# Kernel optimization log

Hardware: AMD Instinct MI355X
Metric: run time of the kernel (lower is better)

Reference implementation:

```python
import jax, jax.numpy as jnp
import numpy as np

WINDOW = 12  # fixed half-window from the original module


def setup_inputs() -> dict:
    key = jax.random.key(0)
    ks = jax.random.split(key, 8)
    B, S, G, H = 8, 512, 16, 128
    Da, Dm = 8 * H, 2 * H
    att = jax.random.normal(ks[0], (B, S, Da), jnp.float32)
    mod = jax.random.normal(ks[1], (B, S, Dm), jnp.float32)
    W_att = jax.random.normal(ks[2], (3 * Da,), jnp.float32) * 0.02
    b_att = jax.random.normal(ks[3], (1,), jnp.float32) * 0.02
    W_mod = jax.random.normal(ks[4], (3 * Dm,), jnp.float32) * 0.02
    b_mod = jax.random.normal(ks[5], (1,), jnp.float32) * 0.02
    q_enc = jax.random.normal(ks[6], (B, 30, Dm), jnp.float32)
    gap_indices = jax.random.randint(ks[7], (B, G), 0, S)
    mask = jnp.ones((B, S), jnp.int32)
    q_mask = jnp.ones((B, 30), jnp.int32)
    return dict(att=att, mod=mod, W_att=W_att, b_att=b_att, W_mod=W_mod,
                b_mod=b_mod, q_enc=q_enc, gap_indices=gap_indices,
                mask=mask, q_mask=q_mask)


def _pools(x, maskf, wmf):
    # x: [B,S,D]; maskf: [B,S] float; wmf: [B,G-1,S] float window masks
    # gap 0: full-sequence pooling (max is unmasked, avg divides by mask sum -- faithful)
    max0 = jnp.max(x, axis=1)                                   # [B,D]
    avg0 = jnp.sum(x, axis=1) / jnp.sum(maskf, axis=1, keepdims=True)
    p0 = jnp.concatenate([max0, avg0], axis=-1)[:, None, :]      # [B,1,2D]
    # remaining gaps: masked windowed max/avg (masked entries zeroed, as in torch)
    s = jnp.einsum('bgs,bsd->bgd', wmf, x)                       # windowed sums
    cnt = jnp.sum(wmf, axis=2, keepdims=True)                    # [B,G-1,1]
    avg = s / cnt
    mx = jnp.max(x[:, None, :, :] * wmf[:, :, :, None], axis=2)  # [B,G-1,D]
    return jnp.concatenate([p0, jnp.concatenate([mx, avg], axis=-1)], axis=1)


def reference(att, mod, W_att, b_att, W_mod, b_mod, q_enc, gap_indices, mask, q_mask):
    B, S, _ = mod.shape
    bidx = jnp.arange(B)[:, None]
    att_gaps = att[bidx, gap_indices]   # [B,G,Da]
    mod_gaps = mod[bidx, gap_indices]   # [B,G,Dm]

    maskf = mask.astype(jnp.float32)
    gaps_rest = gap_indices[:, 1:]      # [B,G-1]
    idx = jnp.arange(S)
    wm = ((idx[None, None, :] >= gaps_rest[:, :, None] - WINDOW)
          & (idx[None, None, :] <= gaps_rest[:, :, None] + WINDOW)
          & (mask[:, None, :] > 0))
    wmf = wm.astype(jnp.float32)        # [B,G-1,S]

    pools_att = _pools(att, maskf, wmf)  # [B,G,2*Da]
    pools_mod = _pools(mod, maskf, wmf)  # [B,G,2*Dm]

    att_cat = jnp.concatenate([att_gaps, pools_att], axis=-1)  # [B,G,3*Da]
    mod_cat = jnp.concatenate([mod_gaps, pools_mod], axis=-1)  # [B,G,3*Dm]

    logits = (jnp.einsum('bgd,d->bg', att_cat, W_att) + b_att
              + jnp.einsum('bgd,d->bg', mod_cat, W_mod) + b_mod)
    return logits  # [B,G]
```

## Files before the change

### kernel.cpp

```cpp
#include <hip/hip_runtime.h>
#include <hip/hip_bf16.h>
#include <math.h>

#define B 8
#define S 512
#define G 16
#define DA 1024
#define DM 256
#define WIN 12
#define NCHUNK 32
#define ROWS (S / NCHUNK)
#define DTOT (DA + DM)
#define NW 8
#define RPW (ROWS / NW)

__inline__ __device__ float4 fmax4(float4 a, float4 b) {
    return make_float4(fmaxf(a.x, b.x), fmaxf(a.y, b.y),
                       fmaxf(a.z, b.z), fmaxf(a.w, b.w));
}
__inline__ __device__ float dot4(float4 a, float4 b) {
    return a.x * b.x + a.y * b.y + a.z * b.z + a.w * b.w;
}

__inline__ __device__ float4 blockReduceSum4_16(float4 v, float4* sh) {
    int lane = threadIdx.x & 63, w = threadIdx.x >> 6;
#pragma unroll
    for (int o = 32; o > 0; o >>= 1) {
        v.x += __shfl_xor(v.x, o, 64);
        v.y += __shfl_xor(v.y, o, 64);
        v.z += __shfl_xor(v.z, o, 64);
        v.w += __shfl_xor(v.w, o, 64);
    }
    __syncthreads();
    if (lane == 0) sh[w] = v;
    __syncthreads();
    float4 r = sh[0];
#pragma unroll
    for (int ww = 1; ww < 16; ++ww) {
        r.x += sh[ww].x; r.y += sh[ww].y; r.z += sh[ww].z; r.w += sh[ww].w;
    }
    return r;
}

__inline__ __device__ float blockReduceSum_16(float v, float* sh) {
    int lane = threadIdx.x & 63, w = threadIdx.x >> 6;
#pragma unroll
    for (int o = 32; o > 0; o >>= 1) v += __shfl_xor(v, o, 64);
    __syncthreads();
    if (lane == 0) sh[w] = v;
    __syncthreads();
    float r = sh[0];
#pragma unroll
    for (int ww = 1; ww < 16; ++ww) r += sh[ww];
    return r;
}

__global__ __launch_bounds__(512) void k_fused(
    const float* __restrict__ att, const float* __restrict__ mod,
    const float* __restrict__ Wa, const float* __restrict__ Wm,
    float* __restrict__ proj0a, float* __restrict__ proj2a,
    float* __restrict__ proj0m, float* __restrict__ proj2m,
    float* __restrict__ pmax)
{
    __shared__ float part[NW][DTOT];
    const int ch = blockIdx.x, b = blockIdx.y;
    const int t = threadIdx.x, lane = t & 63, w = t >> 6;

    const float4* W0 = (const float4*)Wa;
    const float4* W2 = (const float4*)(Wa + 2 * DA);
    float4 w0[4], w2[4];
#pragma unroll
    for (int k = 0; k < 4; ++k) {
        w0[k] = W0[lane + 64 * k];
        w2[k] = W2[lane + 64 * k];
    }
    const float4 wq0 = ((const float4*)Wm)[lane];
    const float4 wq2 = ((const float4*)(Wm + 2 * DM))[lane];

    float4 amax[4], mmax;
#pragma unroll
    for (int k = 0; k < 4; ++k)
        amax[k] = make_float4(-INFINITY, -INFINITY, -INFINITY, -INFINITY);
    mmax = make_float4(-INFINITY, -INFINITY, -INFINITY, -INFINITY);

    const int srow0 = ch * ROWS + w * RPW;
#pragma unroll
    for (int r = 0; r < RPW; ++r) {
        const int row = b * S + srow0 + r;
        const float4* arow = (const float4*)(att + (size_t)row * DA);
        float p0 = 0.f, p2 = 0.f;
#pragma unroll
        for (int k = 0; k < 4; ++k) {
            float4 va = arow[lane + 64 * k];
            p0 += dot4(va, w0[k]);
            p2 += dot4(va, w2[k]);
            amax[k] = fmax4(amax[k], va);
        }
        float4 vm = ((const float4*)(mod + (size_t)row * DM))[lane];
        float q0 = dot4(vm, wq0);
        float q2 = dot4(vm, wq2);
        mmax = fmax4(mmax, vm);

#pragma unroll
        for (int o = 32; o > 0; o >>= 1) {
            p0 += __shfl_xor(p0, o, 64);
            p2 += __shfl_xor(p2, o, 64);
            q0 += __shfl_xor(q0, o, 64);
            q2 += __shfl_xor(q2, o, 64);
        }
        if (lane == 0) {
            proj0a[row] = p0;
            proj2a[row] = p2;
            proj0m[row] = q0;
            proj2m[row] = q2;
        }
    }

    float4* pr = (float4*)&part[w][0];
#pragma unroll
    for (int k = 0; k < 4; ++k) pr[lane + 64 * k] = amax[k];
    ((float4*)&part[w][DA])[lane] = mmax;
    __syncthreads();

    for (int d = t; d < DTOT; d += 512) {
        float m = part[0][d];
#pragma unroll
        for (int ww = 1; ww < NW; ++ww) m = fmaxf(m, part[ww][d]);
        pmax[((size_t)b * NCHUNK + ch) * DTOT + d] = m;
    }
}

__global__ __launch_bounds__(1024) void k_final(
    const float* __restrict__ att, const float* __restrict__ mod,
    const float* __restrict__ Wa, const float* __restrict__ Wm,
    const float* __restrict__ ba, const float* __restrict__ bm,
    const int* __restrict__ gidx, const int* __restrict__ mask,
    const float* __restrict__ proj0a, const float* __restrict__ proj2a,
    const float* __restrict__ proj0m, const float* __restrict__ proj2m,
    const float* __restrict__ pmax,
    float* __restrict__ out)
{
    __shared__ float4 s4v[16];
    __shared__ float s16[16];
    __shared__ float4 pA[4][256];
    __shared__ float  pM[4][256];
    const int g = blockIdx.x, b = blockIdx.y, t = threadIdx.x;
    const int gi = gidx[b * G + g];

    if (g == 0) {
        float sa = 0.f, sm = 0.f, cm = 0.f;
        for (int s = t; s < S; s += 1024) {
            sa += proj2a[b * S + s];
            sm += proj2m[b * S + s];
            cm += (float)mask[b * S + s];
        }
        float gm = 0.f;
        for (int d = t; d < DTOT; d += 1024) {
            float m = -INFINITY;
#pragma unroll
            for (int ch = 0; ch < NCHUNK; ++ch)
                m = fmaxf(m, pmax[((size_t)b * NCHUNK + ch) * DTOT + d]);
            float wgt = (d < DA) ? Wa[DA + d] : Wm[DM + (d - DA)];
            gm += wgt * m;
        }
        float4 r = blockReduceSum4_16(make_float4(sa, sm, cm, gm), s4v);
        if (t == 0) {
            float res = proj0a[b * S + gi] + proj0m[b * S + gi] + r.w +
                        r.x / r.z + r.y / r.z + ba[0] + bm[0];
            out[b * G + 0] = res;
        }
    } else {
        int lo = gi - WIN; if (lo < 0) lo = 0;
        int hi = gi + WIN; if (hi > S - 1) hi = S - 1;

        const int sb = t >> 8;
        const int dt = t & 255;

        float4 m4 = make_float4(0.f, 0.f, 0.f, 0.f);
        float mm = 0.f, sa = 0.f, sm = 0.f, cn = 0.f;
        const float4* a4 = (const float4*)att;
        for (int s = lo + sb; s <= hi; s += 4) {
            if (mask[b * S + s] > 0) {
                float4 v = a4[(size_t)(b * S + s) * (DA / 4) + dt];
                m4 = fmax4(m4, v);
                mm = fmaxf(mm, mod[(size_t)(b * S + s) * DM + dt]);
                if (dt == 0) {
                    sa += proj2a[b * S + s];
                    sm += proj2m[b * S + s];
                    cn += 1.f;
                }
            }
        }
        pA[sb][dt] = m4;
        pM[sb][dt] = mm;
        __syncthreads();

        float pa = 0.f, pm = 0.f;
        if (t < 256) {
            float4 mm4 = fmax4(fmax4(pA[0][t], pA[1][t]),
                               fmax4(pA[2][t], pA[3][t]));
            float mmm = fmaxf(fmaxf(pM[0][t], pM[1][t]),
                              fmaxf(pM[2][t], pM[3][t]));
            const float4* W1a4 = (const float4*)(Wa + DA);
            pa = dot4(mm4, W1a4[t]);
            pm = Wm[DM + t] * mmm;
        }
        float4 r = blockReduceSum4_16(make_float4(pa, pm, sa, sm), s4v);
        cn = blockReduceSum_16(cn, s16);
        if (t == 0) {
            float res = proj0a[b * S + gi] + proj0m[b * S + gi] +
                        r.x + r.y + r.z / cn + r.w / cn + ba[0] + bm[0];
            out[b * G + g] = res;
        }
    }
}

extern "C" void kernel_launch(void* const* d_in, const int* in_sizes, int n_in,
                              void* d_out, int out_size, void* d_ws, size_t ws_size,
                              hipStream_t stream) {
    const float* att  = (const float*)d_in[0];
    const float* mod  = (const float*)d_in[1];
    const float* Wa   = (const float*)d_in[2];
    const float* ba   = (const float*)d_in[3];
    const float* Wm   = (const float*)d_in[4];
    const float* bm   = (const float*)d_in[5];
    const int* gidx   = (const int*)d_in[7];
    const int* mask   = (const int*)d_in[8];
    float* out = (float*)d_out;

    float* ws     = (float*)d_ws;
    float* proj0a = ws;
    float* proj2a = proj0a + B * S;
    float* proj0m = proj2a + B * S;
    float* proj2m = proj0m + B * S;
    float* pmax   = proj2m + B * S;

    k_fused<<<dim3(NCHUNK, B), 512, 0, stream>>>(att, mod, Wa, Wm,
                                                 proj0a, proj2a, proj0m, proj2m,
                                                 pmax);
    k_final<<<dim3(G, B), 1024, 0, stream>>>(att, mod, Wa, Wm, ba, bm, gidx, mask,
                                             proj0a, proj2a, proj0m, proj2m,
                                             pmax, out);
}
```

Measured before the change: 18.87 us.

## Merge two kernels into one cooperative launch with a grid-wide sync

Fuses the per-chunk projection/max kernel and the per-gap finalization kernel into one cooperative kernel separated by a grid sync, so the second launch and its gap go away. The second phase now runs on 128 of the 256 blocks with 512 threads each and reuses the shared buffer, reorganizing the window max by wavefront rows. This adds the cost of a grid-wide barrier and requires all 256 blocks to be co-resident, which the cooperative launch needs.

```diff
diff --git a/kernel.cpp b/kernel.cpp
--- a/kernel.cpp
+++ b/kernel.cpp
@@ -1,6 +1,8 @@
 #include <hip/hip_runtime.h>
-#include <hip/hip_bf16.h>
+#include <hip/hip_cooperative_groups.h>
 #include <math.h>
+
+namespace cg = cooperative_groups;
 
 #define B 8
 #define S 512
@@ -22,7 +24,7 @@
     return a.x * b.x + a.y * b.y + a.z * b.z + a.w * b.w;
 }
 
-__inline__ __device__ float4 blockReduceSum4_16(float4 v, float4* sh) {
+__inline__ __device__ float4 blockReduceSum4_8(float4 v, float4* sh) {
     int lane = threadIdx.x & 63, w = threadIdx.x >> 6;
 #pragma unroll
     for (int o = 32; o > 0; o >>= 1) {
@@ -36,126 +38,108 @@
     __syncthreads();
     float4 r = sh[0];
 #pragma unroll
-    for (int ww = 1; ww < 16; ++ww) {
+    for (int ww = 1; ww < NW; ++ww) {
         r.x += sh[ww].x; r.y += sh[ww].y; r.z += sh[ww].z; r.w += sh[ww].w;
     }
     return r;
 }
 
-__inline__ __device__ float blockReduceSum_16(float v, float* sh) {
-    int lane = threadIdx.x & 63, w = threadIdx.x >> 6;
-#pragma unroll
-    for (int o = 32; o > 0; o >>= 1) v += __shfl_xor(v, o, 64);
-    __syncthreads();
-    if (lane == 0) sh[w] = v;
-    __syncthreads();
-    float r = sh[0];
-#pragma unroll
-    for (int ww = 1; ww < 16; ++ww) r += sh[ww];
-    return r;
-}
-
-__global__ __launch_bounds__(512) void k_fused(
-    const float* __restrict__ att, const float* __restrict__ mod,
-    const float* __restrict__ Wa, const float* __restrict__ Wm,
-    float* __restrict__ proj0a, float* __restrict__ proj2a,
-    float* __restrict__ proj0m, float* __restrict__ proj2m,
-    float* __restrict__ pmax)
-{
-    __shared__ float part[NW][DTOT];
-    const int ch = blockIdx.x, b = blockIdx.y;
-    const int t = threadIdx.x, lane = t & 63, w = t >> 6;
-
-    const float4* W0 = (const float4*)Wa;
-    const float4* W2 = (const float4*)(Wa + 2 * DA);
-    float4 w0[4], w2[4];
-#pragma unroll
-    for (int k = 0; k < 4; ++k) {
-        w0[k] = W0[lane + 64 * k];
-        w2[k] = W2[lane + 64 * k];
-    }
-    const float4 wq0 = ((const float4*)Wm)[lane];
-    const float4 wq2 = ((const float4*)(Wm + 2 * DM))[lane];
-
-    float4 amax[4], mmax;
-#pragma unroll
-    for (int k = 0; k < 4; ++k)
-        amax[k] = make_float4(-INFINITY, -INFINITY, -INFINITY, -INFINITY);
-    mmax = make_float4(-INFINITY, -INFINITY, -INFINITY, -INFINITY);
-
-    const int srow0 = ch * ROWS + w * RPW;
-#pragma unroll
-    for (int r = 0; r < RPW; ++r) {
-        const int row = b * S + srow0 + r;
-        const float4* arow = (const float4*)(att + (size_t)row * DA);
-        float p0 = 0.f, p2 = 0.f;
-#pragma unroll
-        for (int k = 0; k < 4; ++k) {
-            float4 va = arow[lane + 64 * k];
-            p0 += dot4(va, w0[k]);
-            p2 += dot4(va, w2[k]);
-            amax[k] = fmax4(amax[k], va);
-        }
-        float4 vm = ((const float4*)(mod + (size_t)row * DM))[lane];
-        float q0 = dot4(vm, wq0);
-        float q2 = dot4(vm, wq2);
-        mmax = fmax4(mmax, vm);
-
-#pragma unroll
-        for (int o = 32; o > 0; o >>= 1) {
-            p0 += __shfl_xor(p0, o, 64);
-            p2 += __shfl_xor(p2, o, 64);
-            q0 += __shfl_xor(q0, o, 64);
-            q2 += __shfl_xor(q2, o, 64);
-        }
-        if (lane == 0) {
-            proj0a[row] = p0;
-            proj2a[row] = p2;
-            proj0m[row] = q0;
-            proj2m[row] = q2;
-        }
-    }
-
-    float4* pr = (float4*)&part[w][0];
-#pragma unroll
-    for (int k = 0; k < 4; ++k) pr[lane + 64 * k] = amax[k];
-    ((float4*)&part[w][DA])[lane] = mmax;
-    __syncthreads();
-
-    for (int d = t; d < DTOT; d += 512) {
-        float m = part[0][d];
-#pragma unroll
-        for (int ww = 1; ww < NW; ++ww) m = fmaxf(m, part[ww][d]);
-        pmax[((size_t)b * NCHUNK + ch) * DTOT + d] = m;
-    }
-}
-
-__global__ __launch_bounds__(1024) void k_final(
+__global__ __launch_bounds__(512) void k_all(
     const float* __restrict__ att, const float* __restrict__ mod,
     const float* __restrict__ Wa, const float* __restrict__ Wm,
     const float* __restrict__ ba, const float* __restrict__ bm,
     const int* __restrict__ gidx, const int* __restrict__ mask,
-    const float* __restrict__ proj0a, const float* __restrict__ proj2a,
-    const float* __restrict__ proj0m, const float* __restrict__ proj2m,
-    const float* __restrict__ pmax,
-    float* __restrict__ out)
+    float* __restrict__ proj0a, float* __restrict__ proj2a,
+    float* __restrict__ proj0m, float* __restrict__ proj2m,
+    float* __restrict__ pmax, float* __restrict__ out)
 {
-    __shared__ float4 s4v[16];
-    __shared__ float s16[16];
-    __shared__ float4 pA[4][256];
-    __shared__ float  pM[4][256];
-    const int g = blockIdx.x, b = blockIdx.y, t = threadIdx.x;
+    __shared__ float part[NW][DTOT];
+    __shared__ float4 s4[NW];
+    const int t = threadIdx.x, lane = t & 63, w = t >> 6;
+
+    {
+        const int ch = blockIdx.x, b = blockIdx.y;
+
+        const float4* W0 = (const float4*)Wa;
+        const float4* W2 = (const float4*)(Wa + 2 * DA);
+        float4 w0[4], w2[4];
+#pragma unroll
+        for (int k = 0; k < 4; ++k) {
+            w0[k] = W0[lane + 64 * k];
+            w2[k] = W2[lane + 64 * k];
+        }
+        const float4 wq0 = ((const float4*)Wm)[lane];
+        const float4 wq2 = ((const float4*)(Wm + 2 * DM))[lane];
+
+        float4 amax[4], mmax;
+#pragma unroll
+        for (int k = 0; k < 4; ++k)
+            amax[k] = make_float4(-INFINITY, -INFINITY, -INFINITY, -INFINITY);
+        mmax = make_float4(-INFINITY, -INFINITY, -INFINITY, -INFINITY);
+
+        const int srow0 = ch * ROWS + w * RPW;
+#pragma unroll
+        for (int r = 0; r < RPW; ++r) {
+            const int row = b * S + srow0 + r;
+            const float4* arow = (const float4*)(att + (size_t)row * DA);
+            float p0 = 0.f, p2 = 0.f;
+#pragma unroll
+            for (int k = 0; k < 4; ++k) {
+                float4 va = arow[lane + 64 * k];
+                p0 += dot4(va, w0[k]);
+                p2 += dot4(va, w2[k]);
+                amax[k] = fmax4(amax[k], va);
+            }
+            float4 vm = ((const float4*)(mod + (size_t)row * DM))[lane];
+            float q0 = dot4(vm, wq0);
+            float q2 = dot4(vm, wq2);
+            mmax = fmax4(mmax, vm);
+
+#pragma unroll
+            for (int o = 32; o > 0; o >>= 1) {
+                p0 += __shfl_xor(p0, o, 64);
+                p2 += __shfl_xor(p2, o, 64);
+                q0 += __shfl_xor(q0, o, 64);
+                q2 += __shfl_xor(q2, o, 64);
+            }
+            if (lane == 0) {
+                proj0a[row] = p0;
+                proj2a[row] = p2;
+                proj0m[row] = q0;
+                proj2m[row] = q2;
+            }
+        }
+
+        float4* pr = (float4*)&part[w][0];
+#pragma unroll
+        for (int k = 0; k < 4; ++k) pr[lane + 64 * k] = amax[k];
+        ((float4*)&part[w][DA])[lane] = mmax;
+        __syncthreads();
+
+        for (int d = t; d < DTOT; d += 512) {
+            float m = part[0][d];
+#pragma unroll
+            for (int ww = 1; ww < NW; ++ww) m = fmaxf(m, part[ww][d]);
+            pmax[((size_t)b * NCHUNK + ch) * DTOT + d] = m;
+        }
+    }
+
+    cg::this_grid().sync();
+
+    const int bid = blockIdx.y * NCHUNK + blockIdx.x;
+    if (bid >= B * G) return;
+    const int g = bid & (G - 1), b = bid >> 4;
     const int gi = gidx[b * G + g];
 
     if (g == 0) {
         float sa = 0.f, sm = 0.f, cm = 0.f;
-        for (int s = t; s < S; s += 1024) {
+        for (int s = t; s < S; s += 512) {
             sa += proj2a[b * S + s];
             sm += proj2m[b * S + s];
             cm += (float)mask[b * S + s];
         }
         float gm = 0.f;
-        for (int d = t; d < DTOT; d += 1024) {
+        for (int d = t; d < DTOT; d += 512) {
             float m = -INFINITY;
 #pragma unroll
             for (int ch = 0; ch < NCHUNK; ++ch)
@@ -163,54 +147,55 @@
             float wgt = (d < DA) ? Wa[DA + d] : Wm[DM + (d - DA)];
             gm += wgt * m;
         }
-        float4 r = blockReduceSum4_16(make_float4(sa, sm, cm, gm), s4v);
+        float4 r = blockReduceSum4_8(make_float4(sa, sm, cm, gm), s4);
         if (t == 0) {
-            float res = proj0a[b * S + gi] + proj0m[b * S + gi] + r.w +
-                        r.x / r.z + r.y / r.z + ba[0] + bm[0];
-            out[b * G + 0] = res;
+            out[b * G + 0] = proj0a[b * S + gi] + proj0m[b * S + gi] + r.w +
+                             r.x / r.z + r.y / r.z + ba[0] + bm[0];
         }
     } else {
         int lo = gi - WIN; if (lo < 0) lo = 0;
         int hi = gi + WIN; if (hi > S - 1) hi = S - 1;
 
-        const int sb = t >> 8;
-        const int dt = t & 255;
-
-        float4 m4 = make_float4(0.f, 0.f, 0.f, 0.f);
-        float mm = 0.f, sa = 0.f, sm = 0.f, cn = 0.f;
-        const float4* a4 = (const float4*)att;
-        for (int s = lo + sb; s <= hi; s += 4) {
+        float4 amax2[4];
+#pragma unroll
+        for (int k = 0; k < 4; ++k) amax2[k] = make_float4(0.f, 0.f, 0.f, 0.f);
+        float4 mmax2 = make_float4(0.f, 0.f, 0.f, 0.f);
+        float sa = 0.f, sm = 0.f, cn = 0.f;
+
+        for (int s = lo + w; s <= hi; s += NW) {
             if (mask[b * S + s] > 0) {
-                float4 v = a4[(size_t)(b * S + s) * (DA / 4) + dt];
-                m4 = fmax4(m4, v);
-                mm = fmaxf(mm, mod[(size_t)(b * S + s) * DM + dt]);
-                if (dt == 0) {
-                    sa += proj2a[b * S + s];
-                    sm += proj2m[b * S + s];
+                const int row = b * S + s;
+                const float4* arow = (const float4*)(att + (size_t)row * DA);
+#pragma unroll
+                for (int k = 0; k < 4; ++k)
+                    amax2[k] = fmax4(amax2[k], arow[lane + 64 * k]);
+                mmax2 = fmax4(mmax2, ((const float4*)(mod + (size_t)row * DM))[lane]);
+                if (lane == 0) {
+                    sa += proj2a[row];
+                    sm += proj2m[row];
                     cn += 1.f;
                 }
             }
         }
-        pA[sb][dt] = m4;
-        pM[sb][dt] = mm;
+
+        float4* pr = (float4*)&part[w][0];
+#pragma unroll
+        for (int k = 0; k < 4; ++k) pr[lane + 64 * k] = amax2[k];
+        ((float4*)&part[w][DA])[lane] = mmax2;
         __syncthreads();
 
-        float pa = 0.f, pm = 0.f;
-        if (t < 256) {
-            float4 mm4 = fmax4(fmax4(pA[0][t], pA[1][t]),
-                               fmax4(pA[2][t], pA[3][t]));
-            float mmm = fmaxf(fmaxf(pM[0][t], pM[1][t]),
-                              fmaxf(pM[2][t], pM[3][t]));
-            const float4* W1a4 = (const float4*)(Wa + DA);
-            pa = dot4(mm4, W1a4[t]);
-            pm = Wm[DM + t] * mmm;
-        }
-        float4 r = blockReduceSum4_16(make_float4(pa, pm, sa, sm), s4v);
-        cn = blockReduceSum_16(cn, s16);
+        float wdot = 0.f;
+        for (int d = t; d < DTOT; d += 512) {
+            float m = part[0][d];
+#pragma unroll
+            for (int ww = 1; ww < NW; ++ww) m = fmaxf(m, part[ww][d]);
+            float wgt = (d < DA) ? Wa[DA + d] : Wm[DM + (d - DA)];
+            wdot += wgt * m;
+        }
+        float4 r = blockReduceSum4_8(make_float4(wdot, sa, sm, cn), s4);
         if (t == 0) {
-            float res = proj0a[b * S + gi] + proj0m[b * S + gi] +
-                        r.x + r.y + r.z / cn + r.w / cn + ba[0] + bm[0];
-            out[b * G + g] = res;
+            out[b * G + g] = proj0a[b * S + gi] + proj0m[b * S + gi] +
+                             r.x + r.y / r.w + r.z / r.w + ba[0] + bm[0];
         }
     }
 }
@@ -235,10 +220,12 @@
     float* proj2m = proj0m + B * S;
     float* pmax   = proj2m + B * S;
 
-    k_fused<<<dim3(NCHUNK, B), 512, 0, stream>>>(att, mod, Wa, Wm,
-                                                 proj0a, proj2a, proj0m, proj2m,
-                                                 pmax);
-    k_final<<<dim3(G, B), 1024, 0, stream>>>(att, mod, Wa, Wm, ba, bm, gidx, mask,
-                                             proj0a, proj2a, proj0m, proj2m,
-                                             pmax, out);
-}
+    void* args[] = {
+        (void*)&att, (void*)&mod, (void*)&Wa, (void*)&Wm,
+        (void*)&ba, (void*)&bm, (void*)&gidx, (void*)&mask,
+        (void*)&proj0a, (void*)&proj2a, (void*)&proj0m, (void*)&proj2m,
+        (void*)&pmax, (void*)&out
+    };
+    hipLaunchCooperativeKernel((void*)k_all, dim3(NCHUNK, B), dim3(512),
+                               args, 0, stream);
+}
```

New measurement: 52.46 us. 178% more time.
